# Kernel tuning notes

Measured on AMD Instinct MI355X. Metric: run time of the kernel, lower is better.

## Reference

```python
import jax, jax.numpy as jnp
import numpy as np

B, L1, L2, DIM_HID = 32, 64, 64, 256
FEAT = 2 * DIM_HID  # per-sequence feature dim; pair dim = 4*dim_hid


def setup_inputs() -> dict:
    key = jax.random.key(0)
    k1, k2, k3, k4, k5, k6 = jax.random.split(key, 6)
    x1 = jax.random.normal(k1, (B, L1, FEAT), dtype=jnp.float32)
    x2 = jax.random.normal(k2, (B, L2, FEAT), dtype=jnp.float32)
    # lengths in [1, L]; force max length so torch's dynamic max_len == L1*L2
    seq_lens1 = jax.random.randint(k3, (B,), 1, L1 + 1).at[0].set(L1)
    seq_lens2 = jax.random.randint(k4, (B,), 1, L2 + 1).at[0].set(L2)
    W = jax.random.normal(k5, (DIM_HID, 4 * DIM_HID), dtype=jnp.float32) * (1.0 / np.sqrt(4 * DIM_HID))
    b = jax.random.normal(k6, (DIM_HID,), dtype=jnp.float32) * 0.01
    return {"x1": x1, "seq_lens1": seq_lens1, "x2": x2, "seq_lens2": seq_lens2, "W": W, "b": b}


def reference(x1, seq_lens1, x2, seq_lens2, W, b):
    # Faithful to torch: for each sample, all (i,j) pairs with i<sl1, j<sl2 get
    # feature concat(x1[i], x2[j]); remaining rows (up to max_len = L1*L2) are
    # zero-padded BEFORE Linear+ReLU, so they contribute relu(b) to the sum.
    # Linear on concat == split GEMM: x1 @ W[:, :F].T + x2 @ W[:, F:].T + b,
    # which avoids materializing the [B, L1*L2, 4h] pair tensor.
    y1 = jnp.einsum('bif,hf->bih', x1, W[:, :FEAT])  # [B, L1, H]
    y2 = jnp.einsum('bjf,hf->bjh', x2, W[:, FEAT:])  # [B, L2, H]
    mask = (jnp.arange(L1)[None, :] < seq_lens1[:, None])[:, :, None] & \
           (jnp.arange(L2)[None, :] < seq_lens2[:, None])[:, None, :]  # [B, L1, L2]
    z = jnp.where(mask[..., None], y1[:, :, None, :] + y2[:, None, :, :] + b, b)
    y = jax.nn.relu(z)  # [B, L1, L2, H]; dropout is identity (eval / p handled)
    denom = (seq_lens1 * seq_lens2).astype(x1.dtype)[:, None]
    return y.sum(axis=(1, 2)) / denom
```

## Files before the change

kernel.cpp:

```cpp
#include <hip/hip_runtime.h>

#define BB 32
#define LL 64
#define HH 256
#define FF 512
#define WSTRIDE 1024
#define HT 16
#define BK 128
#define LSTR 136
#define YSTR 17

typedef float float4v __attribute__((ext_vector_type(4)));
typedef short short8  __attribute__((ext_vector_type(8)));

static __device__ __forceinline__ unsigned int cvt_pk_bf16(float lo, float hi) {
    unsigned int r;
    asm("v_cvt_pk_bf16_f32 %0, %1, %2" : "=v"(r) : "v"(lo), "v"(hi));
    return r;
}

static __device__ __forceinline__ short8 load_cvt8(const float* __restrict__ p) {
    const float4 f0 = *(const float4*)p;
    const float4 f1 = *(const float4*)(p + 4);
    union { short8 s; unsigned int u[4]; } o;
    o.u[0] = cvt_pk_bf16(f0.x, f0.y);
    o.u[1] = cvt_pk_bf16(f0.z, f0.w);
    o.u[2] = cvt_pk_bf16(f1.x, f1.y);
    o.u[3] = cvt_pk_bf16(f1.z, f1.w);
    return o.s;
}

__global__ __launch_bounds__(256)
void fused_kernel(const float* __restrict__ x1,
                  const float* __restrict__ x2,
                  const float* __restrict__ W,
                  const int* __restrict__ s1p,
                  const int* __restrict__ s2p,
                  const float* __restrict__ bias,
                  float* __restrict__ out) {
    const int b  = blockIdx.x;
    const int h0 = blockIdx.y * HT;

    __shared__ __align__(16) unsigned char smem[43520];
    unsigned short (*As1)[LSTR] = (unsigned short (*)[LSTR])(smem);
    unsigned short (*As2)[LSTR] = (unsigned short (*)[LSTR])(smem + 17408);
    unsigned short (*Bs1)[LSTR] = (unsigned short (*)[LSTR])(smem + 34816);
    unsigned short (*Bs2)[LSTR] = (unsigned short (*)[LSTR])(smem + 39168);
    float (*y1t)[YSTR]     = (float (*)[YSTR])(smem);
    float (*y2t)[YSTR]     = (float (*)[YSTR])(smem + 4352);
    float (*partial)[YSTR] = (float (*)[YSTR])(smem + 8704);

    const int t      = threadIdx.x;
    const int lane   = t & 63;
    const int wid    = t >> 6;
    const int srcSel = wid >> 1;
    const int mrow   = (wid & 1) * 32;
    const int lm     = lane & 15;
    const int quad   = lane >> 4;

    const int r    = t >> 2;  const int kq   = t & 3;
    const int rw   = t >> 4;  const int kq16 = t & 15;

    const float* a1p = x1 + (size_t)(b * LL + r) * FF + kq * 32;
    const float* a2p = x2 + (size_t)(b * LL + r) * FF + kq * 32;
    const float* w1p = W + (size_t)(h0 + rw) * WSTRIDE + kq16 * 8;
    const float* w2p = w1p + FF;

    float4v acc[2];
    acc[0] = (float4v){0.f, 0.f, 0.f, 0.f};
    acc[1] = (float4v){0.f, 0.f, 0.f, 0.f};

    short8 pa1[4], pa2[4], pw1, pw2;
    #pragma unroll
    for (int q = 0; q < 4; ++q) {
        pa1[q] = load_cvt8(a1p + q * 8);
        pa2[q] = load_cvt8(a2p + q * 8);
    }
    pw1 = load_cvt8(w1p);
    pw2 = load_cvt8(w2p);

    const unsigned short (*Ap)[LSTR] = srcSel ? As2 : As1;
    const unsigned short (*Bp)[LSTR] = srcSel ? Bs2 : Bs1;
    const unsigned short* aF0 = &Ap[mrow + lm][quad * 8];
    const unsigned short* aF1 = &Ap[mrow + 16 + lm][quad * 8];
    const unsigned short* bF0 = &Bp[lm][quad * 8];

    for (int kt = 0; kt < FF / BK; ++kt) {
        #pragma unroll
        for (int q = 0; q < 4; ++q) {
            *(short8*)&As1[r][kq * 32 + q * 8] = pa1[q];
            *(short8*)&As2[r][kq * 32 + q * 8] = pa2[q];
        }
        *(short8*)&Bs1[rw][kq16 * 8] = pw1;
        *(short8*)&Bs2[rw][kq16 * 8] = pw2;
        __syncthreads();

        if (kt + 1 < FF / BK) {
            const int ko = (kt + 1) * BK;
            #pragma unroll
            for (int q = 0; q < 4; ++q) {
                pa1[q] = load_cvt8(a1p + ko + q * 8);
                pa2[q] = load_cvt8(a2p + ko + q * 8);
            }
            pw1 = load_cvt8(w1p + ko);
            pw2 = load_cvt8(w2p + ko);
        }

        #pragma unroll
        for (int ks = 0; ks < 4; ++ks) {
            const short8 a0 = *(const short8*)(aF0 + ks * 32);
            const short8 a1 = *(const short8*)(aF1 + ks * 32);
            const short8 b0 = *(const short8*)(bF0 + ks * 32);
            acc[0] = __builtin_amdgcn_mfma_f32_16x16x32_bf16(a0, b0, acc[0], 0, 0, 0);
            acc[1] = __builtin_amdgcn_mfma_f32_16x16x32_bf16(a1, b0, acc[1], 0, 0, 0);
        }
        __syncthreads();
    }

    {
        float (*yt)[YSTR] = srcSel ? y2t : y1t;
        const float bv = srcSel ? bias[h0 + lm] : 0.0f;
        #pragma unroll
        for (int im = 0; im < 2; ++im)
            #pragma unroll
            for (int j = 0; j < 4; ++j)
                yt[mrow + im * 16 + quad * 4 + j][lm] = acc[im][j] + bv;
    }
    __syncthreads();

    const int n1 = s1p[b];
    const int n2 = s2p[b];
    const int h  = t & 15;
    const int ic = t >> 4;

    float r1[4];
    #pragma unroll
    for (int ii = 0; ii < 4; ++ii) {
        const int i = ic * 4 + ii;
        r1[ii] = (i < n1) ? y1t[i][h] : -1e30f;
    }

    float ac[4] = {0.f, 0.f, 0.f, 0.f};
    int j = 0;
    for (; j + 4 <= n2; j += 4) {
        const float v0 = y2t[j][h];
        const float v1 = y2t[j + 1][h];
        const float v2 = y2t[j + 2][h];
        const float v3 = y2t[j + 3][h];
        #pragma unroll
        for (int ii = 0; ii < 4; ++ii) {
            ac[ii] += fmaxf(r1[ii] + v0, 0.f);
            ac[ii] += fmaxf(r1[ii] + v1, 0.f);
            ac[ii] += fmaxf(r1[ii] + v2, 0.f);
            ac[ii] += fmaxf(r1[ii] + v3, 0.f);
        }
    }
    for (; j < n2; ++j) {
        const float v0 = y2t[j][h];
        #pragma unroll
        for (int ii = 0; ii < 4; ++ii)
            ac[ii] += fmaxf(r1[ii] + v0, 0.f);
    }
    partial[ic][h] = (ac[0] + ac[1]) + (ac[2] + ac[3]);
    __syncthreads();

    if (t < HT) {
        float s = 0.f;
        #pragma unroll
        for (int ic2 = 0; ic2 < 16; ++ic2)
            s += partial[ic2][t];
        const float denom = (float)(n1 * n2);
        const float pad = (float)(LL * LL) - denom;
        out[b * HH + h0 + t] = (s + pad * fmaxf(bias[h0 + t], 0.f)) / denom;
    }
}

extern "C" void kernel_launch(void* const* d_in, const int* in_sizes, int n_in,
                              void* d_out, int out_size, void* d_ws, size_t ws_size,
                              hipStream_t stream) {
    const float* x1 = (const float*)d_in[0];
    const int*   s1 = (const int*)d_in[1];
    const float* x2 = (const float*)d_in[2];
    const int*   s2 = (const int*)d_in[3];
    const float* W  = (const float*)d_in[4];
    const float* b  = (const float*)d_in[5];
    float* out = (float*)d_out;
    (void)d_ws; (void)ws_size;

    fused_kernel<<<dim3(BB, HH / HT), 256, 0, stream>>>(x1, x2, W, s1, s2, b, out);
}
```

Before: 86.45 us.

## Precompute bf16 swizzled inputs and stream tiles via direct global-to-LDS loads

A separate conversion kernel now writes x1, x2 and W as bf16 into the workspace, XOR-swizzled so the layout matches the LDS fragment reads. The main kernel then fetches tiles with global_load_lds into double-buffered shared memory, replacing the register staging and per-block fp32-to-bf16 conversion. This halves global read traffic in the GEMM and removes the redundant conversions, since each block previously converted the same x rows and W rows again. The cost is an extra kernel launch plus a full write and re-read of the bf16 copies through memory.

After: 74.45 us. 13.9% less time.

```diff
diff --git a/kernel.cpp b/kernel.cpp
--- a/kernel.cpp
+++ b/kernel.cpp
@@ -7,8 +7,16 @@
 #define WSTRIDE 1024
 #define HT 16
 #define BK 128
-#define LSTR 136
 #define YSTR 17
+
+#define NX1 (BB * LL * FF)
+#define NX  (2 * NX1)
+#define NW  (HH * WSTRIDE)
+#define NTOT (NX + NW)
+
+#define ATILE_SH 8192
+#define BTILE_SH 2048
+#define BUF_SH   (2 * ATILE_SH + 2 * BTILE_SH)
 
 typedef float float4v __attribute__((ext_vector_type(4)));
 typedef short short8  __attribute__((ext_vector_type(8)));
@@ -19,21 +27,45 @@
     return r;
 }
 
-static __device__ __forceinline__ short8 load_cvt8(const float* __restrict__ p) {
-    const float4 f0 = *(const float4*)p;
-    const float4 f1 = *(const float4*)(p + 4);
+static __device__ __forceinline__ void gl16(const unsigned short* g, unsigned short* l) {
+    __builtin_amdgcn_global_load_lds(
+        (const __attribute__((address_space(1))) void*)(const void*)g,
+        (__attribute__((address_space(3))) void*)(void*)l,
+        16, 0, 0);
+}
+
+__global__ __launch_bounds__(256)
+void convert_kernel(const float* __restrict__ x1,
+                    const float* __restrict__ x2,
+                    const float* __restrict__ W,
+                    unsigned short* __restrict__ xb,
+                    unsigned short* __restrict__ Wb) {
+    const int idx = (blockIdx.x * 256 + threadIdx.x) * 8;
+    const float* src;
+    unsigned short* dst;
+    if (idx < NX) {
+        src = (idx < NX1) ? (x1 + idx) : (x2 + (idx - NX1));
+        const int r7 = (idx >> 9) & 7;
+        dst = xb + (idx ^ (r7 << 3));
+    } else {
+        const int rel = idx - NX;
+        src = W + rel;
+        const int r7 = (rel >> 10) & 7;
+        dst = Wb + (rel ^ (r7 << 3));
+    }
+    const float4 f0 = *(const float4*)src;
+    const float4 f1 = *(const float4*)(src + 4);
     union { short8 s; unsigned int u[4]; } o;
     o.u[0] = cvt_pk_bf16(f0.x, f0.y);
     o.u[1] = cvt_pk_bf16(f0.z, f0.w);
     o.u[2] = cvt_pk_bf16(f1.x, f1.y);
     o.u[3] = cvt_pk_bf16(f1.z, f1.w);
-    return o.s;
+    *(short8*)dst = o.s;
 }
 
 __global__ __launch_bounds__(256)
-void fused_kernel(const float* __restrict__ x1,
-                  const float* __restrict__ x2,
-                  const float* __restrict__ W,
+void fused_kernel(const unsigned short* __restrict__ xb,
+                  const unsigned short* __restrict__ Wb,
                   const int* __restrict__ s1p,
                   const int* __restrict__ s2p,
                   const float* __restrict__ bias,
@@ -41,14 +73,10 @@
     const int b  = blockIdx.x;
     const int h0 = blockIdx.y * HT;
 
-    __shared__ __align__(16) unsigned char smem[43520];
-    unsigned short (*As1)[LSTR] = (unsigned short (*)[LSTR])(smem);
-    unsigned short (*As2)[LSTR] = (unsigned short (*)[LSTR])(smem + 17408);
-    unsigned short (*Bs1)[LSTR] = (unsigned short (*)[LSTR])(smem + 34816);
-    unsigned short (*Bs2)[LSTR] = (unsigned short (*)[LSTR])(smem + 39168);
+    __shared__ __align__(16) unsigned short smem[2 * BUF_SH];
     float (*y1t)[YSTR]     = (float (*)[YSTR])(smem);
-    float (*y2t)[YSTR]     = (float (*)[YSTR])(smem + 4352);
-    float (*partial)[YSTR] = (float (*)[YSTR])(smem + 8704);
+    float (*y2t)[YSTR]     = (float (*)[YSTR])((char*)smem + 4352);
+    float (*partial)[YSTR] = (float (*)[YSTR])((char*)smem + 8704);
 
     const int t      = threadIdx.x;
     const int lane   = t & 63;
@@ -58,59 +86,53 @@
     const int lm     = lane & 15;
     const int quad   = lane >> 4;
 
-    const int r    = t >> 2;  const int kq   = t & 3;
-    const int rw   = t >> 4;  const int kq16 = t & 15;
-
-    const float* a1p = x1 + (size_t)(b * LL + r) * FF + kq * 32;
-    const float* a2p = x2 + (size_t)(b * LL + r) * FF + kq * 32;
-    const float* w1p = W + (size_t)(h0 + rw) * WSTRIDE + kq16 * 8;
-    const float* w2p = w1p + FF;
+    const int srow = t >> 4;
+    const int scol = (t & 15) * 8;
+
+    const unsigned short* a1base = xb +       (size_t)(b * LL + srow) * FF + scol;
+    const unsigned short* a2base = xb + NX1 + (size_t)(b * LL + srow) * FF + scol;
+    const unsigned short* w1base = Wb + (size_t)(h0 + srow) * WSTRIDE + scol;
+    const unsigned short* w2base = w1base + FF;
 
     float4v acc[2];
     acc[0] = (float4v){0.f, 0.f, 0.f, 0.f};
     acc[1] = (float4v){0.f, 0.f, 0.f, 0.f};
 
-    short8 pa1[4], pa2[4], pw1, pw2;
-    #pragma unroll
-    for (int q = 0; q < 4; ++q) {
-        pa1[q] = load_cvt8(a1p + q * 8);
-        pa2[q] = load_cvt8(a2p + q * 8);
-    }
-    pw1 = load_cvt8(w1p);
-    pw2 = load_cvt8(w2p);
-
-    const unsigned short (*Ap)[LSTR] = srcSel ? As2 : As1;
-    const unsigned short (*Bp)[LSTR] = srcSel ? Bs2 : Bs1;
-    const unsigned short* aF0 = &Ap[mrow + lm][quad * 8];
-    const unsigned short* aF1 = &Ap[mrow + 16 + lm][quad * 8];
-    const unsigned short* bF0 = &Bp[lm][quad * 8];
+    const int xm  = (lm & 7) << 3;
+    const int qb  = (quad * 8) ^ (xm & 0x18);
+    const int x20 = xm & 0x20;
+
+    auto issue = [&](int kt, int bsel) {
+        unsigned short* Lb = smem + bsel * BUF_SH;
+        const int ko = kt * BK;
+        #pragma unroll
+        for (int q = 0; q < 4; ++q) {
+            gl16(a1base + (size_t)q * (16 * FF) + ko, Lb + q * 2048 + wid * 512);
+            gl16(a2base + (size_t)q * (16 * FF) + ko, Lb + ATILE_SH + q * 2048 + wid * 512);
+        }
+        gl16(w1base + ko, Lb + 2 * ATILE_SH + wid * 512);
+        gl16(w2base + ko, Lb + 2 * ATILE_SH + BTILE_SH + wid * 512);
+    };
+
+    issue(0, 0);
+    __syncthreads();
 
     for (int kt = 0; kt < FF / BK; ++kt) {
-        #pragma unroll
-        for (int q = 0; q < 4; ++q) {
-            *(short8*)&As1[r][kq * 32 + q * 8] = pa1[q];
-            *(short8*)&As2[r][kq * 32 + q * 8] = pa2[q];
-        }
-        *(short8*)&Bs1[rw][kq16 * 8] = pw1;
-        *(short8*)&Bs2[rw][kq16 * 8] = pw2;
-        __syncthreads();
-
-        if (kt + 1 < FF / BK) {
-            const int ko = (kt + 1) * BK;
-            #pragma unroll
-            for (int q = 0; q < 4; ++q) {
-                pa1[q] = load_cvt8(a1p + ko + q * 8);
-                pa2[q] = load_cvt8(a2p + ko + q * 8);
-            }
-            pw1 = load_cvt8(w1p + ko);
-            pw2 = load_cvt8(w2p + ko);
-        }
+        if (kt + 1 < FF / BK) issue(kt + 1, (kt + 1) & 1);
+
+        const unsigned short* Lb = smem + (kt & 1) * BUF_SH;
+        const unsigned short* A  = Lb + (srcSel ? ATILE_SH : 0);
+        const unsigned short* Bt = Lb + 2 * ATILE_SH + (srcSel ? BTILE_SH : 0);
+        const unsigned short* pA0 = A + (mrow + lm) * 128 + qb;
+        const unsigned short* pA1 = pA0 + 16 * 128;
+        const unsigned short* pB  = Bt + lm * 128 + qb;
 
         #pragma unroll
         for (int ks = 0; ks < 4; ++ks) {
-            const short8 a0 = *(const short8*)(aF0 + ks * 32);
-            const short8 a1 = *(const short8*)(aF1 + ks * 32);
-            const short8 b0 = *(const short8*)(bF0 + ks * 32);
+            const int kof = (ks * 32) ^ x20;
+            const short8 a0 = *(const short8*)(pA0 + kof);
+            const short8 a1 = *(const short8*)(pA1 + kof);
+            const short8 b0 = *(const short8*)(pB + kof);
             acc[0] = __builtin_amdgcn_mfma_f32_16x16x32_bf16(a0, b0, acc[0], 0, 0, 0);
             acc[1] = __builtin_amdgcn_mfma_f32_16x16x32_bf16(a1, b0, acc[1], 0, 0, 0);
         }
@@ -185,7 +207,10 @@
     const float* W  = (const float*)d_in[4];
     const float* b  = (const float*)d_in[5];
     float* out = (float*)d_out;
-    (void)d_ws; (void)ws_size;
-
-    fused_kernel<<<dim3(BB, HH / HT), 256, 0, stream>>>(x1, x2, W, s1, s2, b, out);
-}
+
+    unsigned short* xb = (unsigned short*)d_ws;
+    unsigned short* Wb = xb + NX;
+
+    convert_kernel<<<NTOT / (256 * 8), 256, 0, stream>>>(x1, x2, W, xb, Wb);
+    fused_kernel<<<dim3(BB, HH / HT), 256, 0, stream>>>(xb, Wb, s1, s2, b, out);
+}
```

## Stream fp32 tiles directly into swizzled double-buffered LDS via global_load_lds

Applied to the files above, without the earlier changes.

Operands are no longer loaded into registers, converted to bf16 and written to LDS. Instead, fp32 tiles of x1, x2 and W are copied straight from global memory into LDS with 16-byte global_load_lds, using an XOR-swizzled layout and two buffers with K-tile size 64. Conversion to bf16 now happens after the LDS reads, just before each MFMA. The goal is to remove register staging and VGPR pressure and to overlap the next tile's copy with compute. In exchange, the LDS footprint roughly doubles, which can limit resident blocks per CU, and correctness depends on the DMA writes being complete before the barriers.

Result: faster. 76.93 us (-11.0%).

```diff
diff --git a/kernel.cpp b/kernel.cpp
--- a/kernel.cpp
+++ b/kernel.cpp
@@ -6,9 +6,15 @@
 #define FF 512
 #define WSTRIDE 1024
 #define HT 16
-#define BK 128
-#define LSTR 136
+#define BK 64
+#define NKT (FF / BK)
 #define YSTR 17
+
+#define A1OFF 0
+#define A2OFF 16384
+#define W1OFF 32768
+#define W2OFF 36864
+#define BUFB  40960
 
 typedef float float4v __attribute__((ext_vector_type(4)));
 typedef short short8  __attribute__((ext_vector_type(8)));
@@ -19,15 +25,19 @@
     return r;
 }
 
-static __device__ __forceinline__ short8 load_cvt8(const float* __restrict__ p) {
-    const float4 f0 = *(const float4*)p;
-    const float4 f1 = *(const float4*)(p + 4);
+static __device__ __forceinline__ short8 cvt8(float4 lo, float4 hi) {
     union { short8 s; unsigned int u[4]; } o;
-    o.u[0] = cvt_pk_bf16(f0.x, f0.y);
-    o.u[1] = cvt_pk_bf16(f0.z, f0.w);
-    o.u[2] = cvt_pk_bf16(f1.x, f1.y);
-    o.u[3] = cvt_pk_bf16(f1.z, f1.w);
+    o.u[0] = cvt_pk_bf16(lo.x, lo.y);
+    o.u[1] = cvt_pk_bf16(lo.z, lo.w);
+    o.u[2] = cvt_pk_bf16(hi.x, hi.y);
+    o.u[3] = cvt_pk_bf16(hi.z, hi.w);
     return o.s;
+}
+
+static __device__ __forceinline__ void gl16(const float* g, void* l) {
+    __builtin_amdgcn_global_load_lds(
+        (const __attribute__((address_space(1))) void*)(const void*)g,
+        (__attribute__((address_space(3))) void*)l, 16, 0, 0);
 }
 
 __global__ __launch_bounds__(256)
@@ -41,11 +51,7 @@
     const int b  = blockIdx.x;
     const int h0 = blockIdx.y * HT;
 
-    __shared__ __align__(16) unsigned char smem[43520];
-    unsigned short (*As1)[LSTR] = (unsigned short (*)[LSTR])(smem);
-    unsigned short (*As2)[LSTR] = (unsigned short (*)[LSTR])(smem + 17408);
-    unsigned short (*Bs1)[LSTR] = (unsigned short (*)[LSTR])(smem + 34816);
-    unsigned short (*Bs2)[LSTR] = (unsigned short (*)[LSTR])(smem + 39168);
+    __shared__ __align__(16) unsigned char smem[2 * BUFB];
     float (*y1t)[YSTR]     = (float (*)[YSTR])(smem);
     float (*y2t)[YSTR]     = (float (*)[YSTR])(smem + 4352);
     float (*partial)[YSTR] = (float (*)[YSTR])(smem + 8704);
@@ -58,59 +64,59 @@
     const int lm     = lane & 15;
     const int quad   = lane >> 4;
 
-    const int r    = t >> 2;  const int kq   = t & 3;
-    const int rw   = t >> 4;  const int kq16 = t & 15;
+    const int srow = t >> 4;
+    const int sg   = (t & 15) ^ (srow & 7);
 
-    const float* a1p = x1 + (size_t)(b * LL + r) * FF + kq * 32;
-    const float* a2p = x2 + (size_t)(b * LL + r) * FF + kq * 32;
-    const float* w1p = W + (size_t)(h0 + rw) * WSTRIDE + kq16 * 8;
-    const float* w2p = w1p + FF;
+    const float* a1g = x1 + (size_t)(b * LL + srow) * FF + sg * 4;
+    const float* a2g = x2 + (size_t)(b * LL + srow) * FF + sg * 4;
+    const float* w1g = W + (size_t)(h0 + srow) * WSTRIDE + sg * 4;
+    const float* w2g = w1g + FF;
 
     float4v acc[2];
     acc[0] = (float4v){0.f, 0.f, 0.f, 0.f};
     acc[1] = (float4v){0.f, 0.f, 0.f, 0.f};
 
-    short8 pa1[4], pa2[4], pw1, pw2;
-    #pragma unroll
-    for (int q = 0; q < 4; ++q) {
-        pa1[q] = load_cvt8(a1p + q * 8);
-        pa2[q] = load_cvt8(a2p + q * 8);
-    }
-    pw1 = load_cvt8(w1p);
-    pw2 = load_cvt8(w2p);
+    const int m     = lm & 7;
+    const int offLo = (((quad * 2)     ^ m) * 16);
+    const int offHi = (((quad * 2 + 1) ^ m) * 16);
+    const int aRowOff = (srcSel ? A2OFF : A1OFF) + (mrow + lm) * 256;
+    const int bRowOff = (srcSel ? W2OFF : W1OFF) + lm * 256;
 
-    const unsigned short (*Ap)[LSTR] = srcSel ? As2 : As1;
-    const unsigned short (*Bp)[LSTR] = srcSel ? Bs2 : Bs1;
-    const unsigned short* aF0 = &Ap[mrow + lm][quad * 8];
-    const unsigned short* aF1 = &Ap[mrow + 16 + lm][quad * 8];
-    const unsigned short* bF0 = &Bp[lm][quad * 8];
-
-    for (int kt = 0; kt < FF / BK; ++kt) {
+    auto issue = [&](int kt, int bsel) {
+        unsigned char* Lb = smem + bsel * BUFB;
+        const int ko = kt * BK;
         #pragma unroll
         for (int q = 0; q < 4; ++q) {
-            *(short8*)&As1[r][kq * 32 + q * 8] = pa1[q];
-            *(short8*)&As2[r][kq * 32 + q * 8] = pa2[q];
+            gl16(a1g + ko + (size_t)q * (16 * FF), Lb + A1OFF + q * 4096 + wid * 1024);
+            gl16(a2g + ko + (size_t)q * (16 * FF), Lb + A2OFF + q * 4096 + wid * 1024);
         }
-        *(short8*)&Bs1[rw][kq16 * 8] = pw1;
-        *(short8*)&Bs2[rw][kq16 * 8] = pw2;
-        __syncthreads();
+        gl16(w1g + ko, Lb + W1OFF + wid * 1024);
+        gl16(w2g + ko, Lb + W2OFF + wid * 1024);
+    };
 
-        if (kt + 1 < FF / BK) {
-            const int ko = (kt + 1) * BK;
-            #pragma unroll
-            for (int q = 0; q < 4; ++q) {
-                pa1[q] = load_cvt8(a1p + ko + q * 8);
-                pa2[q] = load_cvt8(a2p + ko + q * 8);
-            }
-            pw1 = load_cvt8(w1p + ko);
-            pw2 = load_cvt8(w2p + ko);
-        }
+    issue(0, 0);
+    __syncthreads();
+
+    for (int kt = 0; kt < NKT; ++kt) {
+        if (kt + 1 < NKT) issue(kt + 1, (kt + 1) & 1);
+
+        const unsigned char* Lb  = smem + (kt & 1) * BUFB;
+        const unsigned char* pA0 = Lb + aRowOff;
+        const unsigned char* pA1 = pA0 + 16 * 256;
+        const unsigned char* pB  = Lb + bRowOff;
 
         #pragma unroll
-        for (int ks = 0; ks < 4; ++ks) {
-            const short8 a0 = *(const short8*)(aF0 + ks * 32);
-            const short8 a1 = *(const short8*)(aF1 + ks * 32);
-            const short8 b0 = *(const short8*)(bF0 + ks * 32);
+        for (int ks = 0; ks < 2; ++ks) {
+            const int kb = ks * 128;
+            const float4 a0lo = *(const float4*)(pA0 + kb + offLo);
+            const float4 a0hi = *(const float4*)(pA0 + kb + offHi);
+            const float4 a1lo = *(const float4*)(pA1 + kb + offLo);
+            const float4 a1hi = *(const float4*)(pA1 + kb + offHi);
+            const float4 blo  = *(const float4*)(pB  + kb + offLo);
+            const float4 bhi  = *(const float4*)(pB  + kb + offHi);
+            const short8 a0 = cvt8(a0lo, a0hi);
+            const short8 a1 = cvt8(a1lo, a1hi);
+            const short8 b0 = cvt8(blo, bhi);
             acc[0] = __builtin_amdgcn_mfma_f32_16x16x32_bf16(a0, b0, acc[0], 0, 0, 0);
             acc[1] = __builtin_amdgcn_mfma_f32_16x16x32_bf16(a1, b0, acc[1], 0, 0, 0);
         }
```
